# Performance work log

Hardware: AMD Instinct MI355X
Metric: run time of the kernel (lower is better)

Reference implementation:

```python
import jax, jax.numpy as jnp
import numpy as np

TEMPERATURE = 1.0

def setup_inputs() -> dict:
    key = jax.random.key(0)
    k1, k2 = jax.random.split(key)
    B, I, O = 256, 1024, 1024
    x = jax.random.normal(k1, (B, I), dtype=jnp.float32)
    # mimic TruncatedNormal(stddev=1/sqrt(input_size)) init
    w = jax.random.normal(k2, (I, O), dtype=jnp.float32) * (1.0 / np.sqrt(I))
    b = jnp.zeros((O,), dtype=jnp.float32)
    return {"x": x, "w": w, "b": b}

def reference(x, w, b):
    # z: [B, I, O] outer product per sample
    z = jnp.einsum('bi,io->bio', x, w)
    n = x.shape[-1]
    # per-output-neuron temperature softmax over the input dim I
    s = jax.nn.softmax(jnp.abs(z) / TEMPERATURE, axis=1)
    out = n * jnp.sum(z * s, axis=1)  # [B, O]
    return out + b
```

## Files before the change

kernel.cpp:

```cpp
#include <hip/hip_runtime.h>

#define BDIM 256
#define IDIM 1024
#define ODIM 1024

#define TILE_OL 2
#define TILE_O (64 * TILE_OL)
#define TILE_B 4
#define NW 8
#define QLEN (IDIM / NW)
#define CHUNK 8
#define NCHUNK (QLEN / CHUNK)

typedef float v2f __attribute__((ext_vector_type(2)));
typedef float v4f __attribute__((ext_vector_type(4)));

#if __has_builtin(__builtin_amdgcn_exp2f)
#define FAST_EXP2(v) __builtin_amdgcn_exp2f(v)
#else
#define FAST_EXP2(v) exp2f(v)
#endif

__global__ __launch_bounds__(512, 4)
void stl_kernel(const float* __restrict__ x,
                const float* __restrict__ w,
                const float* __restrict__ bias,
                float* __restrict__ out) {
  __shared__ float xs[TILE_B][IDIM];
  __shared__ float ps[NW][64][16];

  const int tx = threadIdx.x;
  const int ty = threadIdx.y;
  const int tid = ty * 64 + tx;
  const int o0 = blockIdx.x * TILE_O;
  const int b0 = blockIdx.y * TILE_B;

  const float LOG2E = 1.4426950408889634f;

#pragma unroll
  for (int k = 0; k < 2; ++k) {
    int f = tid + k * 512;
    int row = f >> 8;
    int col = f & 255;
    float4 v = ((const float4*)(x + (size_t)(b0 + row) * IDIM))[col];
    v.x *= LOG2E; v.y *= LOG2E; v.z *= LOG2E; v.w *= LOG2E;
    ((float4*)(&xs[row][0]))[col] = v;
  }
  __syncthreads();

  const int qbase = ty * QLEN;
  const float* wp = w + (size_t)qbase * ODIM + o0 + tx;

  v2f an[TILE_OL][TILE_B], ad[TILE_OL][TILE_B];
#pragma unroll
  for (int s = 0; s < TILE_OL; ++s)
#pragma unroll
    for (int r = 0; r < TILE_B; ++r) { an[s][r] = (v2f){0.f, 0.f}; ad[s][r] = (v2f){0.f, 0.f}; }

  v2f wA0[CHUNK / 2], wA1[CHUNK / 2], wB0[CHUNK / 2], wB1[CHUNK / 2];

#define WLOAD(d0, d1, cc)                                                 \
  {                                                                       \
    const float* wq = wp + (size_t)((cc) * CHUNK) * ODIM;                 \
    _Pragma("unroll")                                                     \
    for (int u = 0; u < CHUNK / 2; ++u) {                                 \
      d0[u].x = wq[(size_t)(2 * u) * ODIM];                               \
      d0[u].y = wq[(size_t)(2 * u + 1) * ODIM];                           \
      d1[u].x = wq[(size_t)(2 * u) * ODIM + 64];                          \
      d1[u].y = wq[(size_t)(2 * u + 1) * ODIM + 64];                      \
    }                                                                     \
  }

#define ROWP(acc_n, acc_d, xpair, wpair)                                  \
  {                                                                       \
    v2f p = (xpair) * (wpair);                              \
    v2f t;                                                                \
    t.x = FAST_EXP2(__builtin_fabsf(p.x));          \
    t.y = FAST_EXP2(__builtin_fabsf(p.y));                                \
    acc_n += p * t;                                         \
    acc_d += t;                                             \
  }

#define LO(xq) __builtin_shufflevector(xq, xq, 0, 1)
#define HI(xq) __builtin_shufflevector(xq, xq, 2, 3)

#define COMPUTE(wc0, wc1, cc)                                             \
  {                                                                       \
    const int jb = qbase + (cc) * CHUNK;                                  \
    _Pragma("unroll")                                                     \
    for (int h = 0; h < 2; ++h) {                                         \
      v4f xq[TILE_B];                                                     \
      _Pragma("unroll")                                                   \
      for (int r = 0; r < TILE_B; ++r)                                    \
        xq[r] = *(const v4f*)(&xs[r][jb + h * 4]);                        \
      _Pragma("unroll")                                                   \
      for (int r = 0; r < TILE_B; ++r) {                                  \
        ROWP(an[0][r], ad[0][r], LO(xq[r]), wc0[h * 2])                   \
        ROWP(an[0][r], ad[0][r], HI(xq[r]), wc0[h * 2 + 1])               \
        ROWP(an[1][r], ad[1][r], LO(xq[r]), wc1[h * 2])                   \
        ROWP(an[1][r], ad[1][r], HI(xq[r]), wc1[h * 2 + 1])               \
      }                                                                   \
    }                                                                     \
  }

  WLOAD(wA0, wA1, 0)
  for (int c = 0; c < NCHUNK; c += 2) {
    WLOAD(wB0, wB1, c + 1)
    COMPUTE(wA0, wA1, c)
    WLOAD(wA0, wA1, (c + 2) & (NCHUNK - 1))
    COMPUTE(wB0, wB1, c + 1)
  }

#pragma unroll
  for (int s = 0; s < TILE_OL; ++s) {
    *(float4*)(&ps[ty][tx][s * 8 + 0]) =
        make_float4(an[s][0].x + an[s][0].y, an[s][1].x + an[s][1].y,
                    an[s][2].x + an[s][2].y, an[s][3].x + an[s][3].y);
    *(float4*)(&ps[ty][tx][s * 8 + 4]) =
        make_float4(ad[s][0].x + ad[s][0].y, ad[s][1].x + ad[s][1].y,
                    ad[s][2].x + ad[s][2].y, ad[s][3].x + ad[s][3].y);
  }
  __syncthreads();

  if (ty == 0) {
    const float LN2 = 0.6931471805599453f;
    const float scale = (float)IDIM * LN2;
#pragma unroll
    for (int s = 0; s < TILE_OL; ++s) {
      float n[4] = {0, 0, 0, 0}, d[4] = {0, 0, 0, 0};
#pragma unroll
      for (int q = 0; q < NW; ++q) {
        float4 a = *(const float4*)(&ps[q][tx][s * 8 + 0]);
        float4 b2 = *(const float4*)(&ps[q][tx][s * 8 + 4]);
        n[0] += a.x; n[1] += a.y; n[2] += a.z; n[3] += a.w;
        d[0] += b2.x; d[1] += b2.y; d[2] += b2.z; d[3] += b2.w;
      }
      const int o = o0 + tx + s * 64;
      const float bo = bias[o];
#pragma unroll
      for (int r = 0; r < 4; ++r)
        out[(size_t)(b0 + r) * ODIM + o] = scale * n[r] / d[r] + bo;
    }
  }
}

extern "C" void kernel_launch(void* const* d_in, const int* in_sizes, int n_in,
                              void* d_out, int out_size, void* d_ws, size_t ws_size,
                              hipStream_t stream) {
  const float* x = (const float*)d_in[0];
  const float* w = (const float*)d_in[1];
  const float* b = (const float*)d_in[2];
  float* out = (float*)d_out;

  dim3 grid(ODIM / TILE_O, BDIM / TILE_B);
  dim3 block(64, NW);
  stl_kernel<<<grid, block, 0, stream>>>(x, w, b, out);
}
```

Before: 90.95 us.

## Pre-transpose x and w into workspace, keep x in registers, broadcast w

A new prep kernel transposes x to [I][B] and rearranges w, pre-scaled by log2e, into per-wave contiguous [segment][O][128] slabs in the workspace. The main kernel keeps 128 x-values per lane in registers and reads w with wave-uniform addresses, so those loads can become scalar or broadcast loads. It loops over 16 outputs per block and reduces across the 8 waves in shared memory. This is meant to remove the shared-memory x reads and the strided w loads, at the cost of an extra kernel launch, a workspace round trip, and high register pressure. The old kernel is kept as a fallback when the workspace is too small.

After: 97.96 us. 7.7% more time.

```diff
diff --git a/kernel.cpp b/kernel.cpp
--- a/kernel.cpp
+++ b/kernel.cpp
@@ -4,16 +4,12 @@
 #define IDIM 1024
 #define ODIM 1024
 
-#define TILE_OL 2
-#define TILE_O (64 * TILE_OL)
-#define TILE_B 4
 #define NW 8
-#define QLEN (IDIM / NW)
-#define CHUNK 8
-#define NCHUNK (QLEN / CHUNK)
+#define QLEN 128
+#define NO 16
+#define NPAIR (QLEN / 2)
 
 typedef float v2f __attribute__((ext_vector_type(2)));
-typedef float v4f __attribute__((ext_vector_type(4)));
 
 #if __has_builtin(__builtin_amdgcn_exp2f)
 #define FAST_EXP2(v) __builtin_amdgcn_exp2f(v)
@@ -21,34 +17,136 @@
 #define FAST_EXP2(v) exp2f(v)
 #endif
 
+__global__ __launch_bounds__(256)
+void prep_kernel(const float* __restrict__ x, const float* __restrict__ w,
+                 float* __restrict__ wS, float* __restrict__ xT) {
+  __shared__ float lt[64][65];
+  const int tid = threadIdx.x;
+  const float LOG2E = 1.4426950408889634f;
+  const int t = blockIdx.x;
+  if (t < 256) {
+    const int i0 = (t >> 4) * 64, o0 = (t & 15) * 64;
+#pragma unroll
+    for (int k = 0; k < 16; ++k) {
+      int idx = tid + k * 256, r = idx >> 6, c = idx & 63;
+      lt[r][c] = LOG2E * w[(size_t)(i0 + r) * ODIM + o0 + c];
+    }
+    __syncthreads();
+#pragma unroll
+    for (int k = 0; k < 16; ++k) {
+      int idx = tid + k * 256, ol = idx >> 6, il = idx & 63;
+      int gi = i0 + il, go = o0 + ol;
+      int e = gi >> 7, ip = gi & 127;
+      wS[(size_t)e * (ODIM * QLEN) + (size_t)go * QLEN + ip] = lt[il][ol];
+    }
+  } else {
+    const int t2 = t - 256;
+    const int i0 = (t2 >> 2) * 64, b0 = (t2 & 3) * 64;
+#pragma unroll
+    for (int k = 0; k < 16; ++k) {
+      int idx = tid + k * 256, r = idx >> 6, c = idx & 63;
+      lt[r][c] = x[(size_t)(b0 + r) * IDIM + i0 + c];
+    }
+    __syncthreads();
+#pragma unroll
+    for (int k = 0; k < 16; ++k) {
+      int idx = tid + k * 256, il = idx >> 6, bl = idx & 63;
+      xT[(size_t)(i0 + il) * BDIM + b0 + bl] = lt[bl][il];
+    }
+  }
+}
+
+__global__ __launch_bounds__(512, 2)
+void stl_main(const float* __restrict__ xT, const float* __restrict__ wS,
+              const float* __restrict__ bias, float* __restrict__ out) {
+  __shared__ float ps[NW][64][2 * NO];
+
+  const int tx = threadIdx.x;
+  const int ty = threadIdx.y;
+  const int o0 = blockIdx.x * NO;
+  const int b0 = blockIdx.y * 64;
+  const int tyu = __builtin_amdgcn_readfirstlane(ty);
+  const int qbase = tyu * QLEN;
+
+  v2f xv[NPAIR];
+#pragma unroll
+  for (int u = 0; u < NPAIR; ++u) {
+    xv[u].x = xT[(size_t)(qbase + 2 * u) * BDIM + b0 + tx];
+    xv[u].y = xT[(size_t)(qbase + 2 * u + 1) * BDIM + b0 + tx];
+  }
+
+  const float* wrow = wS + (size_t)tyu * (ODIM * QLEN) + (size_t)o0 * QLEN;
+
+  for (int o = 0; o < NO; ++o) {
+    const float* wr = wrow + (size_t)o * QLEN;
+    v2f accn = {0.f, 0.f}, accd = {0.f, 0.f};
+#pragma unroll
+    for (int k = 0; k < NPAIR; ++k) {
+      v2f sw;
+      sw.x = wr[2 * k];
+      sw.y = wr[2 * k + 1];
+      v2f p = xv[k] * sw;
+      v2f t;
+      t.x = FAST_EXP2(__builtin_fabsf(p.x));
+      t.y = FAST_EXP2(__builtin_fabsf(p.y));
+      accn += p * t;
+      accd += t;
+    }
+    v2f res;
+    res.x = accn.x + accn.y;
+    res.y = accd.x + accd.y;
+    *(v2f*)&ps[ty][tx][2 * o] = res;
+  }
+  __syncthreads();
+
+  const int tid = ty * 64 + tx;
+  const int b = tid >> 3;
+  const int op = (tid & 7) * 2;
+  float n0 = 0.f, d0 = 0.f, n1 = 0.f, d1 = 0.f;
+#pragma unroll
+  for (int wv = 0; wv < NW; ++wv) {
+    float4 a = *(const float4*)&ps[wv][b][2 * op];
+    n0 += a.x; d0 += a.y; n1 += a.z; d1 += a.w;
+  }
+  const float LN2 = 0.6931471805599453f;
+  const float scale = (float)IDIM * LN2;
+  float2 r;
+  r.x = scale * n0 / d0 + bias[o0 + op];
+  r.y = scale * n1 / d1 + bias[o0 + op + 1];
+  *(float2*)&out[(size_t)(b0 + b) * ODIM + o0 + op] = r;
+}
+
+#define TILE_OL 2
+#define TILE_O (64 * TILE_OL)
+#define TILE_B 4
+#define FQLEN (IDIM / NW)
+#define CHUNK 8
+#define NCHUNK (FQLEN / CHUNK)
+
+typedef float v4f __attribute__((ext_vector_type(4)));
+
 __global__ __launch_bounds__(512, 4)
-void stl_kernel(const float* __restrict__ x,
-                const float* __restrict__ w,
-                const float* __restrict__ bias,
-                float* __restrict__ out) {
+void stl_old(const float* __restrict__ x, const float* __restrict__ w,
+             const float* __restrict__ bias, float* __restrict__ out) {
   __shared__ float xs[TILE_B][IDIM];
   __shared__ float ps[NW][64][16];
 
-  const int tx = threadIdx.x;
-  const int ty = threadIdx.y;
+  const int tx = threadIdx.x, ty = threadIdx.y;
   const int tid = ty * 64 + tx;
   const int o0 = blockIdx.x * TILE_O;
   const int b0 = blockIdx.y * TILE_B;
-
   const float LOG2E = 1.4426950408889634f;
 
 #pragma unroll
   for (int k = 0; k < 2; ++k) {
-    int f = tid + k * 512;
-    int row = f >> 8;
-    int col = f & 255;
+    int f = tid + k * 512, row = f >> 8, col = f & 255;
     float4 v = ((const float4*)(x + (size_t)(b0 + row) * IDIM))[col];
     v.x *= LOG2E; v.y *= LOG2E; v.z *= LOG2E; v.w *= LOG2E;
     ((float4*)(&xs[row][0]))[col] = v;
   }
   __syncthreads();
 
-  const int qbase = ty * QLEN;
+  const int qbase = ty * FQLEN;
   const float* wp = w + (size_t)qbase * ODIM + o0 + tx;
 
   v2f an[TILE_OL][TILE_B], ad[TILE_OL][TILE_B];
@@ -59,32 +157,32 @@
 
   v2f wA0[CHUNK / 2], wA1[CHUNK / 2], wB0[CHUNK / 2], wB1[CHUNK / 2];
 
-#define WLOAD(d0, d1, cc)                                                 \
+#define WLOADF(d0_, d1_, cc)                                              \
   {                                                                       \
     const float* wq = wp + (size_t)((cc) * CHUNK) * ODIM;                 \
     _Pragma("unroll")                                                     \
     for (int u = 0; u < CHUNK / 2; ++u) {                                 \
-      d0[u].x = wq[(size_t)(2 * u) * ODIM];                               \
-      d0[u].y = wq[(size_t)(2 * u + 1) * ODIM];                           \
-      d1[u].x = wq[(size_t)(2 * u) * ODIM + 64];                          \
-      d1[u].y = wq[(size_t)(2 * u + 1) * ODIM + 64];                      \
+      d0_[u].x = wq[(size_t)(2 * u) * ODIM];                              \
+      d0_[u].y = wq[(size_t)(2 * u + 1) * ODIM];                          \
+      d1_[u].x = wq[(size_t)(2 * u) * ODIM + 64];                         \
+      d1_[u].y = wq[(size_t)(2 * u + 1) * ODIM + 64];                     \
     }                                                                     \
   }
 
-#define ROWP(acc_n, acc_d, xpair, wpair)                                  \
+#define ROWPF(acc_n, acc_d, xpair, wpair)                                 \
   {                                                                       \
-    v2f p = (xpair) * (wpair);                              \
+    v2f p = (xpair) * (wpair);                                            \
     v2f t;                                                                \
-    t.x = FAST_EXP2(__builtin_fabsf(p.x));          \
+    t.x = FAST_EXP2(__builtin_fabsf(p.x));                                \
     t.y = FAST_EXP2(__builtin_fabsf(p.y));                                \
-    acc_n += p * t;                                         \
-    acc_d += t;                                             \
-  }
-
-#define LO(xq) __builtin_shufflevector(xq, xq, 0, 1)
-#define HI(xq) __builtin_shufflevector(xq, xq, 2, 3)
-
-#define COMPUTE(wc0, wc1, cc)                                             \
+    acc_n += p * t;                                                       \
+    acc_d += t;                                                           \
+  }
+
+#define LOF(xq) __builtin_shufflevector(xq, xq, 0, 1)
+#define HIF(xq) __builtin_shufflevector(xq, xq, 2, 3)
+
+#define COMPUTEF(wc0, wc1, cc)                                            \
   {                                                                       \
     const int jb = qbase + (cc) * CHUNK;                                  \
     _Pragma("unroll")                                                     \
@@ -95,20 +193,20 @@
         xq[r] = *(const v4f*)(&xs[r][jb + h * 4]);                        \
       _Pragma("unroll")                                                   \
       for (int r = 0; r < TILE_B; ++r) {                                  \
-        ROWP(an[0][r], ad[0][r], LO(xq[r]), wc0[h * 2])                   \
-        ROWP(an[0][r], ad[0][r], HI(xq[r]), wc0[h * 2 + 1])               \
-        ROWP(an[1][r], ad[1][r], LO(xq[r]), wc1[h * 2])                   \
-        ROWP(an[1][r], ad[1][r], HI(xq[r]), wc1[h * 2 + 1])               \
+        ROWPF(an[0][r], ad[0][r], LOF(xq[r]), wc0[h * 2])                 \
+        ROWPF(an[0][r], ad[0][r], HIF(xq[r]), wc0[h * 2 + 1])             \
+        ROWPF(an[1][r], ad[1][r], LOF(xq[r]), wc1[h * 2])                 \
+        ROWPF(an[1][r], ad[1][r], HIF(xq[r]), wc1[h * 2 + 1])             \
       }                                                                   \
     }                                                                     \
   }
 
-  WLOAD(wA0, wA1, 0)
+  WLOADF(wA0, wA1, 0)
   for (int c = 0; c < NCHUNK; c += 2) {
-    WLOAD(wB0, wB1, c + 1)
-    COMPUTE(wA0, wA1, c)
-    WLOAD(wA0, wA1, (c + 2) & (NCHUNK - 1))
-    COMPUTE(wB0, wB1, c + 1)
+    WLOADF(wB0, wB1, c + 1)
+    COMPUTEF(wA0, wA1, c)
+    WLOADF(wA0, wA1, (c + 2) & (NCHUNK - 1))
+    COMPUTEF(wB0, wB1, c + 1)
   }
 
 #pragma unroll
@@ -152,7 +250,19 @@
   const float* b = (const float*)d_in[2];
   float* out = (float*)d_out;
 
-  dim3 grid(ODIM / TILE_O, BDIM / TILE_B);
-  dim3 block(64, NW);
-  stl_kernel<<<grid, block, 0, stream>>>(x, w, b, out);
-}
+  const size_t wS_bytes = (size_t)NW * ODIM * QLEN * sizeof(float);
+  const size_t xT_bytes = (size_t)IDIM * BDIM * sizeof(float);
+
+  if (ws_size >= wS_bytes + xT_bytes) {
+    float* wS = (float*)d_ws;
+    float* xT = (float*)((char*)d_ws + wS_bytes);
+    prep_kernel<<<320, 256, 0, stream>>>(x, w, wS, xT);
+    dim3 grid(ODIM / NO, BDIM / 64);
+    dim3 block(64, NW);
+    stl_main<<<grid, block, 0, stream>>>(xT, wS, b, out);
+  } else {
+    dim3 grid(ODIM / TILE_O, BDIM / TILE_B);
+    dim3 block(64, NW);
+    stl_old<<<grid, block, 0, stream>>>(x, w, b, out);
+  }
+}
```

## Triple-buffer weight prefetch, fully unroll chunk loop, rotate chunk order per wave

Applied to the files above, without the earlier changes.

Replaces the two-buffer weight prefetch with a three-buffer register ring, so loads are issued two chunks ahead, and fully unrolls the chunk loop so buffer indices are compile-time constants. Each wave also starts at a rotated chunk offset, which staggers its LDS reads of x and its global reads of w relative to the other waves in the block. This is meant to hide global load latency and cut LDS bank and channel contention. The cost is higher register pressure, since there are more live weight registers plus a larger unrolled body, and that could lower occupancy under the 512x4 launch bounds.

After: 92.38 us. About the same (+1.6%).

```diff
diff --git a/kernel.cpp b/kernel.cpp
--- a/kernel.cpp
+++ b/kernel.cpp
@@ -4,10 +4,10 @@
 #define IDIM 1024
 #define ODIM 1024
 
+#define NW 8
 #define TILE_OL 2
 #define TILE_O (64 * TILE_OL)
 #define TILE_B 4
-#define NW 8
 #define QLEN (IDIM / NW)
 #define CHUNK 8
 #define NCHUNK (QLEN / CHUNK)
@@ -51,40 +51,43 @@
   const int qbase = ty * QLEN;
   const float* wp = w + (size_t)qbase * ODIM + o0 + tx;
 
+  const int rot = ty * 2;
+#define CID(c) ((((c) + rot)) & (NCHUNK - 1))
+
   v2f an[TILE_OL][TILE_B], ad[TILE_OL][TILE_B];
 #pragma unroll
   for (int s = 0; s < TILE_OL; ++s)
 #pragma unroll
     for (int r = 0; r < TILE_B; ++r) { an[s][r] = (v2f){0.f, 0.f}; ad[s][r] = (v2f){0.f, 0.f}; }
 
-  v2f wA0[CHUNK / 2], wA1[CHUNK / 2], wB0[CHUNK / 2], wB1[CHUNK / 2];
+  v2f wbuf[3][TILE_OL][CHUNK / 2];
 
-#define WLOAD(d0, d1, cc)                                                 \
+#define WLOADI(bi, cc)                                                    \
   {                                                                       \
     const float* wq = wp + (size_t)((cc) * CHUNK) * ODIM;                 \
     _Pragma("unroll")                                                     \
     for (int u = 0; u < CHUNK / 2; ++u) {                                 \
-      d0[u].x = wq[(size_t)(2 * u) * ODIM];                               \
-      d0[u].y = wq[(size_t)(2 * u + 1) * ODIM];                           \
-      d1[u].x = wq[(size_t)(2 * u) * ODIM + 64];                          \
-      d1[u].y = wq[(size_t)(2 * u + 1) * ODIM + 64];                      \
+      wbuf[bi][0][u].x = wq[(size_t)(2 * u) * ODIM];                      \
+      wbuf[bi][0][u].y = wq[(size_t)(2 * u + 1) * ODIM];                  \
+      wbuf[bi][1][u].x = wq[(size_t)(2 * u) * ODIM + 64];                 \
+      wbuf[bi][1][u].y = wq[(size_t)(2 * u + 1) * ODIM + 64];             \
     }                                                                     \
   }
 
-#define ROWP(acc_n, acc_d, xpair, wpair)                                  \
+#define ROWPF(acc_n, acc_d, xpair, wpair)                                 \
   {                                                                       \
-    v2f p = (xpair) * (wpair);                              \
+    v2f p = (xpair) * (wpair);                \
     v2f t;                                                                \
-    t.x = FAST_EXP2(__builtin_fabsf(p.x));          \
+    t.x = FAST_EXP2(__builtin_fabsf(p.x));     \
     t.y = FAST_EXP2(__builtin_fabsf(p.y));                                \
     acc_n += p * t;                                         \
     acc_d += t;                                             \
   }
 
-#define LO(xq) __builtin_shufflevector(xq, xq, 0, 1)
-#define HI(xq) __builtin_shufflevector(xq, xq, 2, 3)
+#define LOF(xq) __builtin_shufflevector(xq, xq, 0, 1)
+#define HIF(xq) __builtin_shufflevector(xq, xq, 2, 3)
 
-#define COMPUTE(wc0, wc1, cc)                                             \
+#define COMPUTEI(bi, cc)                                                  \
   {                                                                       \
     const int jb = qbase + (cc) * CHUNK;                                  \
     _Pragma("unroll")                                                     \
@@ -95,20 +98,20 @@
         xq[r] = *(const v4f*)(&xs[r][jb + h * 4]);                        \
       _Pragma("unroll")                                                   \
       for (int r = 0; r < TILE_B; ++r) {                                  \
-        ROWP(an[0][r], ad[0][r], LO(xq[r]), wc0[h * 2])                   \
-        ROWP(an[0][r], ad[0][r], HI(xq[r]), wc0[h * 2 + 1])               \
-        ROWP(an[1][r], ad[1][r], LO(xq[r]), wc1[h * 2])                   \
-        ROWP(an[1][r], ad[1][r], HI(xq[r]), wc1[h * 2 + 1])               \
+        ROWPF(an[0][r], ad[0][r], LOF(xq[r]), wbuf[bi][0][h * 2])         \
+        ROWPF(an[0][r], ad[0][r], HIF(xq[r]), wbuf[bi][0][h * 2 + 1])     \
+        ROWPF(an[1][r], ad[1][r], LOF(xq[r]), wbuf[bi][1][h * 2])         \
+        ROWPF(an[1][r], ad[1][r], HIF(xq[r]), wbuf[bi][1][h * 2 + 1])     \
       }                                                                   \
     }                                                                     \
   }
 
-  WLOAD(wA0, wA1, 0)
-  for (int c = 0; c < NCHUNK; c += 2) {
-    WLOAD(wB0, wB1, c + 1)
-    COMPUTE(wA0, wA1, c)
-    WLOAD(wA0, wA1, (c + 2) & (NCHUNK - 1))
-    COMPUTE(wB0, wB1, c + 1)
+  WLOADI(0, CID(0))
+  WLOADI(1, CID(1))
+#pragma unroll
+  for (int c = 0; c < NCHUNK; ++c) {
+    if (c + 2 < NCHUNK) WLOADI((c + 2) % 3, CID(c + 2))
+    COMPUTEI(c % 3, CID(c))
   }
 
 #pragma unroll
```
